# Optimization experiments

Hardware: AMD Instinct MI355X
Metric: run time of the kernel (lower is better)

The kernel has to match this reference:

```python
import jax, jax.numpy as jnp
import numpy as np

NEG_INF = -1.0e9


def setup_inputs() -> dict:
    key = jax.random.key(0)
    ks = jax.random.split(key, 8)
    B, H, S, D = 8, 8, 1024, 64
    return {
        "gv_feat": jax.random.normal(ks[0], (B, D), dtype=jnp.float32),
        "query2": jax.random.normal(ks[1], (B, H, S, D), dtype=jnp.float32),
        "key": jax.random.normal(ks[2], (B, H, S, D), dtype=jnp.float32),
        "att_mask": jax.random.randint(ks[3], (B, S), 0, 2, dtype=jnp.int32),
        "value1": jax.random.normal(ks[4], (B, H, S, D), dtype=jnp.float32),
        "value2": jax.random.normal(ks[5], (B, H, S, D), dtype=jnp.float32),
        "W_ch": jax.random.normal(ks[6], (D, D), dtype=jnp.float32) * (1.0 / np.sqrt(D)),
        "b_ch": jnp.zeros((D,), dtype=jnp.float32),
    }


def reference(gv_feat, query2, key, att_mask, value1, value2, W_ch, b_ch):
    # query2/key/value1/value2: [B, H, S, D]; att_mask: [B, S]
    D = query2.shape[-1]
    scaling = D ** (-0.5)
    # spatial attention: masked scaled QK^T softmax
    scores = jnp.einsum("bhqd,bhkd->bhqk", query2, key) * scaling  # [B,H,S,S]
    mask = att_mask[:, None, None, :]  # [B,1,1,S]
    scores = jnp.where(mask == 0, NEG_INF, scores)
    alpha_spatial = jax.nn.softmax(scores, axis=-1)
    attn2 = jnp.einsum("bhqk,bhkd->bhqd", alpha_spatial, value2)  # [B,H,S,D]
    # channel attention: sigmoid-gated linear over elementwise value1*key
    att_map_channel = value1 * key  # [B,H,S,D]
    alpha_channel = jax.nn.sigmoid(
        jnp.einsum("bhsd,ed->bhse", att_map_channel, W_ch) + b_ch
    )
    attn2 = alpha_channel * attn2
    return (gv_feat, attn2)
```

## Files before the change

kernel.cpp:

```cpp
#include <hip/hip_runtime.h>

typedef __attribute__((ext_vector_type(4)))  float f32x4;
typedef __attribute__((ext_vector_type(16))) float f32x16;
typedef __attribute__((ext_vector_type(8)))  short bf16x8;
typedef __attribute__((ext_vector_type(4)))  unsigned u32x4;
typedef __attribute__((ext_vector_type(2)))  unsigned u32x2;

#define NEG_INF_F (-1000000000.0f)

__device__ inline unsigned bfbits(float f) {
    union { float f; unsigned u; } v; v.f = f;
    return (v.u + 0x7fffu + ((v.u >> 16) & 1u)) >> 16;
}
__device__ inline unsigned pkbf(float a, float b) {
    return bfbits(a) | (bfbits(b) << 16);
}

__global__ __launch_bounds__(512) void aoa_attn_kernel(
    const float* __restrict__ gv,
    const float* __restrict__ q2,
    const float* __restrict__ keyp,
    const int*   __restrict__ maskp,
    const float* __restrict__ v1,
    const float* __restrict__ v2,
    const float* __restrict__ W,
    const float* __restrict__ bch,
    float* __restrict__ out)
{
    constexpr int S = 1024, D = 64;
    const int bh  = blockIdx.x;
    const int qt  = blockIdx.y;
    const int b   = bh >> 3;
    const int tid = threadIdx.x;
    const int wid = tid >> 6;
    const int lane = tid & 63;
    const int l31 = lane & 31;
    const int h   = lane >> 5;

    float* out_attn = out + 512;
    if (bh == 0 && qt == 0) out[tid] = gv[tid];

    __shared__ float maskf[S];
    __shared__ short Klds[64][72];
    __shared__ short Vt[64][72];
    __shared__ float Lw[8][32];

    for (int i = tid; i < S; i += 512)
        maskf[i] = maskp[b * S + i] ? 0.0f : NEG_INF_F;

    const size_t base = (size_t)bh * S * D;
    const float* Qp  = q2   + base;
    const float* Kp  = keyp + base;
    const float* V1p = v1   + base;
    const float* V2p = v2   + base;

    const int q0   = qt * 256 + wid * 32;
    const int qrow = q0 + l31;

    bf16x8 bq[4];
    #pragma unroll
    for (int ds = 0; ds < 4; ++ds) {
        const f32x4* p = (const f32x4*)(Qp + (size_t)qrow * D + ds * 16 + h * 8);
        f32x4 x0 = p[0], x1 = p[1];
        u32x4 u = (u32x4){pkbf(x0[0], x0[1]), pkbf(x0[2], x0[3]),
                          pkbf(x1[0], x1[1]), pkbf(x1[2], x1[3])};
        bq[ds] = *(bf16x8*)&u;
    }

    f32x16 acc_o[2];
    #pragma unroll
    for (int dh = 0; dh < 2; ++dh)
        #pragma unroll
        for (int r = 0; r < 16; ++r) acc_o[dh][r] = 0.0f;

    float m_run = -1e30f, l_run = 0.0f;
    const float SC = 0.125f * 1.4426950408889634f;

    const int kk  = tid >> 3;
    const int d0  = (tid & 7) << 3;
    const int dcol = tid & 63;
    const int kr0  = (tid >> 6) << 3;

    f32x4 kA, kB;
    float vv[8];
    {
        const f32x4* src = (const f32x4*)(Kp + (size_t)kk * D + d0);
        kA = src[0]; kB = src[1];
        #pragma unroll
        for (int i = 0; i < 8; ++i) vv[i] = V2p[(size_t)(kr0 + i) * D + dcol];
    }

    for (int t = 0; t < 16; ++t) {
        const int kt = t * 64;
        __syncthreads();
        *(u32x4*)&Klds[kk][d0] = (u32x4){pkbf(kA[0], kA[1]), pkbf(kA[2], kA[3]),
                                         pkbf(kB[0], kB[1]), pkbf(kB[2], kB[3])};
        *(u32x4*)&Vt[dcol][kr0] = (u32x4){pkbf(vv[0], vv[1]), pkbf(vv[2], vv[3]),
                                          pkbf(vv[4], vv[5]), pkbf(vv[6], vv[7])};
        __syncthreads();

        if (t < 15) {
            const int kn = kt + 64;
            const f32x4* src = (const f32x4*)(Kp + (size_t)(kn + kk) * D + d0);
            kA = src[0]; kB = src[1];
            #pragma unroll
            for (int i = 0; i < 8; ++i) vv[i] = V2p[(size_t)(kn + kr0 + i) * D + dcol];
        }

        f32x16 accs[2];
        #pragma unroll
        for (int sub = 0; sub < 2; ++sub) {
            f32x16 a;
            #pragma unroll
            for (int r = 0; r < 16; ++r) a[r] = 0.0f;
            #pragma unroll
            for (int ds = 0; ds < 4; ++ds) {
                bf16x8 ak = *(const bf16x8*)&Klds[sub * 32 + l31][ds * 16 + h * 8];
                a = __builtin_amdgcn_mfma_f32_32x32x16_bf16(ak, bq[ds], a, 0, 0, 0);
            }
            accs[sub] = a;
        }

        float s[32];
        float tmax = -1e30f;
        #pragma unroll
        for (int sub = 0; sub < 2; ++sub)
            #pragma unroll
            for (int g = 0; g < 4; ++g) {
                f32x4 mk = *(const f32x4*)&maskf[kt + sub * 32 + g * 8 + h * 4];
                #pragma unroll
                for (int j = 0; j < 4; ++j) {
                    float val = fmaf(accs[sub][g * 4 + j], SC, mk[j]);
                    s[sub * 16 + g * 4 + j] = val;
                    tmax = fmaxf(tmax, val);
                }
            }
        tmax = fmaxf(tmax, __shfl_xor(tmax, 32));

        if (__any(tmax > m_run + 8.0f)) {
            float mnew = fmaxf(m_run, tmax);
            float r = __builtin_amdgcn_exp2f(m_run - mnew);
            l_run *= r;
            #pragma unroll
            for (int dh = 0; dh < 2; ++dh)
                #pragma unroll
                for (int r2 = 0; r2 < 16; ++r2) acc_o[dh][r2] *= r;
            m_run = mnew;
        }

        float psum = 0.0f;
        unsigned w[16];
        #pragma unroll
        for (int i = 0; i < 16; ++i) {
            float p0 = __builtin_amdgcn_exp2f(s[2 * i]     - m_run);
            float p1 = __builtin_amdgcn_exp2f(s[2 * i + 1] - m_run);
            psum += p0 + p1;
            w[i] = pkbf(p0, p1);
        }
        psum += __shfl_xor(psum, 32);
        l_run += psum;

        #pragma unroll
        for (int sub = 0; sub < 2; ++sub) {
            #pragma unroll
            for (int t2 = 0; t2 < 2; ++t2) {
                const int wb = sub * 8 + t2 * 4;
                u32x2 r0 = __builtin_amdgcn_permlane32_swap(w[wb + 0], w[wb + 2], false, false);
                u32x2 r1 = __builtin_amdgcn_permlane32_swap(w[wb + 1], w[wb + 3], false, false);
                u32x4 ua = (u32x4){r0[0], r1[0], r0[1], r1[1]};
                bf16x8 pa = *(bf16x8*)&ua;
                #pragma unroll
                for (int dh = 0; dh < 2; ++dh) {
                    bf16x8 bv = *(const bf16x8*)&Vt[dh * 32 + l31][sub * 32 + t2 * 16 + h * 8];
                    acc_o[dh] = __builtin_amdgcn_mfma_f32_32x32x16_bf16(pa, bv, acc_o[dh], 0, 0, 0);
                }
            }
        }
    }

    f32x16 acc_g[2];
    #pragma unroll
    for (int eh = 0; eh < 2; ++eh)
        #pragma unroll
        for (int r = 0; r < 16; ++r) acc_g[eh][r] = 0.0f;

    bf16x8 bam[4];
    #pragma unroll
    for (int ds = 0; ds < 4; ++ds) {
        const f32x4* p1 = (const f32x4*)(V1p + (size_t)qrow * D + ds * 16 + h * 8);
        const f32x4* pk = (const f32x4*)(Kp  + (size_t)qrow * D + ds * 16 + h * 8);
        f32x4 a0 = p1[0], a1 = p1[1], c0 = pk[0], c1 = pk[1];
        u32x4 u = (u32x4){pkbf(a0[0] * c0[0], a0[1] * c0[1]), pkbf(a0[2] * c0[2], a0[3] * c0[3]),
                          pkbf(a1[0] * c1[0], a1[1] * c1[1]), pkbf(a1[2] * c1[2], a1[3] * c1[3])};
        bam[ds] = *(bf16x8*)&u;
    }
    #pragma unroll
    for (int eh = 0; eh < 2; ++eh) {
        #pragma unroll
        for (int ds = 0; ds < 4; ++ds) {
            const f32x4* pw = (const f32x4*)(W + (size_t)(eh * 32 + l31) * D + ds * 16 + h * 8);
            f32x4 x0 = pw[0], x1 = pw[1];
            u32x4 u = (u32x4){pkbf(x0[0], x0[1]), pkbf(x0[2], x0[3]),
                              pkbf(x1[0], x1[1]), pkbf(x1[2], x1[3])};
            bf16x8 bw = *(bf16x8*)&u;
            acc_g[eh] = __builtin_amdgcn_mfma_f32_32x32x16_bf16(bam[ds], bw, acc_g[eh], 0, 0, 0);
        }
    }

    Lw[wid][l31] = 1.0f / l_run;
    const float bv0 = bch[l31], bv1 = bch[32 + l31];
    #pragma unroll
    for (int dh = 0; dh < 2; ++dh) {
        const float bc = dh ? bv1 : bv0;
        #pragma unroll
        for (int r = 0; r < 16; ++r) {
            const int ql = (r & 3) + 8 * (r >> 2) + 4 * h;
            float invl = Lw[wid][ql];
            float o = acc_o[dh][r] * invl;
            float z = acc_g[dh][r] + bc;
            float gate = 1.0f / (1.0f + __expf(-z));
            out_attn[base + (size_t)(q0 + ql) * D + dh * 32 + l31] = o * gate;
        }
    }
}

extern "C" void kernel_launch(void* const* d_in, const int* in_sizes, int n_in,
                              void* d_out, int out_size, void* d_ws, size_t ws_size,
                              hipStream_t stream) {
    const float* gv   = (const float*)d_in[0];
    const float* q2   = (const float*)d_in[1];
    const float* keyp = (const float*)d_in[2];
    const int*   mask = (const int*)  d_in[3];
    const float* v1   = (const float*)d_in[4];
    const float* v2   = (const float*)d_in[5];
    const float* W    = (const float*)d_in[6];
    const float* bch  = (const float*)d_in[7];
    float* out = (float*)d_out;

    dim3 grid(64, 4);
    aoa_attn_kernel<<<grid, 512, 0, stream>>>(gv, q2, keyp, mask, v1, v2, W, bch, out);
}
```

Measured before the change: 49.00 us.

## Double-buffer K/V tiles in LDS and raise wave priority around MFMAs

Splits the K and V LDS staging into two buffers, so the next tile is written into the alternate buffer after the PV MFMAs. This removes one of the two block barriers per iteration and lets global loads overlap compute. It also wraps the MFMA sections in s_setprio and swaps the hand-written bf16 rounding for the library conversion. The cost is double the LDS for K/V, which may lower occupancy, and the library conversion may produce different instructions.

```diff
diff --git a/kernel.cpp b/kernel.cpp
--- a/kernel.cpp
+++ b/kernel.cpp
@@ -1,4 +1,5 @@
 #include <hip/hip_runtime.h>
+#include <hip/hip_bf16.h>
 
 typedef __attribute__((ext_vector_type(4)))  float f32x4;
 typedef __attribute__((ext_vector_type(16))) float f32x16;
@@ -8,12 +9,11 @@
 
 #define NEG_INF_F (-1000000000.0f)
 
-__device__ inline unsigned bfbits(float f) {
-    union { float f; unsigned u; } v; v.f = f;
-    return (v.u + 0x7fffu + ((v.u >> 16) & 1u)) >> 16;
-}
 __device__ inline unsigned pkbf(float a, float b) {
-    return bfbits(a) | (bfbits(b) << 16);
+    union { __hip_bfloat16 h; unsigned short u; } x, y;
+    x.h = __float2bfloat16(a);
+    y.h = __float2bfloat16(b);
+    return (unsigned)x.u | ((unsigned)y.u << 16);
 }
 
 __global__ __launch_bounds__(512) void aoa_attn_kernel(
@@ -41,8 +41,8 @@
     if (bh == 0 && qt == 0) out[tid] = gv[tid];
 
     __shared__ float maskf[S];
-    __shared__ short Klds[64][72];
-    __shared__ short Vt[64][72];
+    __shared__ short Klds[2][64][72];
+    __shared__ short Vt[2][64][72];
     __shared__ float Lw[8][32];
 
     for (int i = tid; i < S; i += 512)
@@ -76,8 +76,8 @@
     float m_run = -1e30f, l_run = 0.0f;
     const float SC = 0.125f * 1.4426950408889634f;
 
-    const int kk  = tid >> 3;
-    const int d0  = (tid & 7) << 3;
+    const int kk   = tid >> 3;
+    const int d0   = (tid & 7) << 3;
     const int dcol = tid & 63;
     const int kr0  = (tid >> 6) << 3;
 
@@ -89,25 +89,25 @@
         #pragma unroll
         for (int i = 0; i < 8; ++i) vv[i] = V2p[(size_t)(kr0 + i) * D + dcol];
     }
+    *(u32x4*)&Klds[0][kk][d0] = (u32x4){pkbf(kA[0], kA[1]), pkbf(kA[2], kA[3]),
+                                        pkbf(kB[0], kB[1]), pkbf(kB[2], kB[3])};
+    *(u32x4*)&Vt[0][dcol][kr0] = (u32x4){pkbf(vv[0], vv[1]), pkbf(vv[2], vv[3]),
+                                         pkbf(vv[4], vv[5]), pkbf(vv[6], vv[7])};
+    int cur = 0;
 
     for (int t = 0; t < 16; ++t) {
         const int kt = t * 64;
         __syncthreads();
-        *(u32x4*)&Klds[kk][d0] = (u32x4){pkbf(kA[0], kA[1]), pkbf(kA[2], kA[3]),
-                                         pkbf(kB[0], kB[1]), pkbf(kB[2], kB[3])};
-        *(u32x4*)&Vt[dcol][kr0] = (u32x4){pkbf(vv[0], vv[1]), pkbf(vv[2], vv[3]),
-                                          pkbf(vv[4], vv[5]), pkbf(vv[6], vv[7])};
-        __syncthreads();
 
         if (t < 15) {
-            const int kn = kt + 64;
-            const f32x4* src = (const f32x4*)(Kp + (size_t)(kn + kk) * D + d0);
+            const f32x4* src = (const f32x4*)(Kp + (size_t)(kt + 64 + kk) * D + d0);
             kA = src[0]; kB = src[1];
             #pragma unroll
-            for (int i = 0; i < 8; ++i) vv[i] = V2p[(size_t)(kn + kr0 + i) * D + dcol];
+            for (int i = 0; i < 8; ++i) vv[i] = V2p[(size_t)(kt + 64 + kr0 + i) * D + dcol];
         }
 
         f32x16 accs[2];
+        __builtin_amdgcn_s_setprio(1);
         #pragma unroll
         for (int sub = 0; sub < 2; ++sub) {
             f32x16 a;
@@ -115,11 +115,12 @@
             for (int r = 0; r < 16; ++r) a[r] = 0.0f;
             #pragma unroll
             for (int ds = 0; ds < 4; ++ds) {
-                bf16x8 ak = *(const bf16x8*)&Klds[sub * 32 + l31][ds * 16 + h * 8];
+                bf16x8 ak = *(const bf16x8*)&Klds[cur][sub * 32 + l31][ds * 16 + h * 8];
                 a = __builtin_amdgcn_mfma_f32_32x32x16_bf16(ak, bq[ds], a, 0, 0, 0);
             }
             accs[sub] = a;
         }
+        __builtin_amdgcn_s_setprio(0);
 
         float s[32];
         float tmax = -1e30f;
@@ -160,6 +161,7 @@
         psum += __shfl_xor(psum, 32);
         l_run += psum;
 
+        __builtin_amdgcn_s_setprio(1);
         #pragma unroll
         for (int sub = 0; sub < 2; ++sub) {
             #pragma unroll
@@ -171,11 +173,20 @@
                 bf16x8 pa = *(bf16x8*)&ua;
                 #pragma unroll
                 for (int dh = 0; dh < 2; ++dh) {
-                    bf16x8 bv = *(const bf16x8*)&Vt[dh * 32 + l31][sub * 32 + t2 * 16 + h * 8];
+                    bf16x8 bv = *(const bf16x8*)&Vt[cur][dh * 32 + l31][sub * 32 + t2 * 16 + h * 8];
                     acc_o[dh] = __builtin_amdgcn_mfma_f32_32x32x16_bf16(pa, bv, acc_o[dh], 0, 0, 0);
                 }
             }
         }
+        __builtin_amdgcn_s_setprio(0);
+
+        if (t < 15) {
+            *(u32x4*)&Klds[cur ^ 1][kk][d0] = (u32x4){pkbf(kA[0], kA[1]), pkbf(kA[2], kA[3]),
+                                                      pkbf(kB[0], kB[1]), pkbf(kB[2], kB[3])};
+            *(u32x4*)&Vt[cur ^ 1][dcol][kr0] = (u32x4){pkbf(vv[0], vv[1]), pkbf(vv[2], vv[3]),
+                                                       pkbf(vv[4], vv[5]), pkbf(vv[6], vv[7])};
+        }
+        cur ^= 1;
     }
 
     f32x16 acc_g[2];
@@ -208,6 +219,7 @@
     }
 
     Lw[wid][l31] = 1.0f / l_run;
+    __builtin_amdgcn_wave_barrier();
     const float bv0 = bch[l31], bv1 = bch[32 + l31];
     #pragma unroll
     for (int dh = 0; dh < 2; ++dh) {
```

Result: no change. 48.15 us (-1.7%).
